# Kernel optimization log

Hardware: AMD Instinct MI355X
Metric: run time of the kernel (lower is better)

## Reference

```python
import jax, jax.numpy as jnp
import numpy as np

N_NODES = 100000
N_EDGES = 1700000  # 1.6M random edges + 100k self-loops (dgl.add_self_loop)
HID = 128
N_GRAPHS = 64
N_CLASSES = 10
T_STEPS = 5


def setup_inputs() -> dict:
    key = jax.random.key(0)
    ks = jax.random.split(key, 12)
    m = jax.random.normal(ks[0], (N_NODES,), dtype=jnp.float32)
    n_rand = N_EDGES - N_NODES
    src_r = jax.random.randint(ks[1], (n_rand,), 0, N_NODES)
    dst_r = jax.random.randint(ks[2], (n_rand,), 0, N_NODES)
    loops = jnp.arange(N_NODES)
    src = jnp.concatenate([src_r, loops])
    dst = jnp.concatenate([dst_r, loops])
    graph_ids = jnp.sort(jax.random.randint(ks[3], (N_NODES,), 0, N_GRAPHS))
    s = 0.05
    W_e = jax.random.normal(ks[4], (HID, HID), dtype=jnp.float32) * s
    b_e = jnp.zeros((HID,), dtype=jnp.float32)
    W_ih = jax.random.normal(ks[5], (3 * HID, HID), dtype=jnp.float32) * s
    b_ih = jnp.zeros((3 * HID,), dtype=jnp.float32)
    W_hh = jax.random.normal(ks[6], (3 * HID, HID), dtype=jnp.float32) * s
    b_hh = jnp.zeros((3 * HID,), dtype=jnp.float32)
    W_cls = jax.random.normal(ks[7], (N_CLASSES, HID), dtype=jnp.float32) * s
    b_cls = jnp.zeros((N_CLASSES,), dtype=jnp.float32)
    return {"m": m, "W_e": W_e, "b_e": b_e, "W_ih": W_ih, "b_ih": b_ih,
            "W_hh": W_hh, "b_hh": b_hh, "W_cls": W_cls, "b_cls": b_cls,
            "src": src, "dst": dst, "graph_ids": graph_ids, "n_graphs": N_GRAPHS}


def _gated_graph_forward(m, W_e, b_e, W_ih, b_ih, W_hh, b_hh, W_cls, b_cls,
                         src, dst, graph_ids, n_graphs):
    n_nodes = m.shape[0]
    hid = W_e.shape[0]
    # h = ndata['m'].view(-1,1), zero-padded to out_feats (DGL GatedGraphConv)
    h = jnp.zeros((n_nodes, hid), dtype=m.dtype).at[:, 0].set(m)
    for _ in range(T_STEPS):
        # single edge type: a[v] = sum_{(u,v) in E} W_e h[u] + b_e
        msg = (h @ W_e.T + b_e)[src]                       # [E, H]
        a = jax.ops.segment_sum(msg, dst, num_segments=n_nodes)
        # torch.nn.GRUCell(a, h); gate order: r, z, n
        gi = a @ W_ih.T + b_ih
        gh = h @ W_hh.T + b_hh
        i_r, i_z, i_n = jnp.split(gi, 3, axis=-1)
        h_r, h_z, h_n = jnp.split(gh, 3, axis=-1)
        r = jax.nn.sigmoid(i_r + h_r)
        z = jax.nn.sigmoid(i_z + h_z)
        n = jnp.tanh(i_n + r * h_n)
        h = (1.0 - z) * n + z * h
    h = jax.nn.relu(h)
    # dgl.mean_nodes: per-graph mean over nodes
    sums = jax.ops.segment_sum(h, graph_ids, num_segments=n_graphs)
    cnt = jax.ops.segment_sum(jnp.ones((n_nodes,), h.dtype), graph_ids,
                              num_segments=n_graphs)
    hg = sums / jnp.maximum(cnt, 1.0)[:, None]             # [G, H]
    return hg @ W_cls.T + b_cls                            # [G, C]


def reference(m, W_e, b_e, W_ih, b_ih, W_hh, b_hh, W_cls, b_cls,
              src, dst, graph_ids, n_graphs):
    return _gated_graph_forward(m, W_e, b_e, W_ih, b_ih, W_hh, b_hh,
                                W_cls, b_cls, src, dst, graph_ids, n_graphs)
```

## Files before the change

kernel.cpp:

```cpp
#include <hip/hip_runtime.h>

#define HID 128
#define G3  384
#define TSTEPS 5
#define BSHIFT 9
#define BNODES (1 << BSHIFT)
#define MAXBUK 256
#define PART_EPB 8192

typedef unsigned int  uint;
typedef unsigned short ushort;

typedef float  f32x4  __attribute__((ext_vector_type(4)));
typedef __bf16 bf16x8 __attribute__((ext_vector_type(8)));

union B8u { uint4 u; bf16x8 b; ushort s[8]; };

static __device__ inline ushort f2bf(float f) {
  uint u = __float_as_uint(f);
  uint r = u + 0x7fffu + ((u >> 16) & 1u);
  return (ushort)(r >> 16);
}
static __device__ inline float bf2f(ushort s) {
  return __uint_as_float(((uint)s) << 16);
}

__global__ __launch_bounds__(128) void k_weights(
    const float* __restrict__ W_e, const float* __restrict__ b_e,
    const float* __restrict__ W_ih, const float* __restrict__ W_hh,
    ushort* __restrict__ Wcomb, ushort* __restrict__ Whh16, float* __restrict__ bvec,
    ushort* __restrict__ Wc0, ushort* __restrict__ Wh0)
{
  int j = blockIdx.x, t = threadIdx.x;
  if (j < G3) {
    __shared__ float row[HID];
    row[t] = W_ih[j * HID + t];
    __syncthreads();
    float acc = 0.f;
    for (int k = 0; k < HID; ++k) acc = fmaf(row[k], W_e[k * HID + t], acc);
    Wcomb[j * HID + t] = f2bf(acc);
    if (t == 0) {
      Wc0[j] = f2bf(acc);
      float b = 0.f;
      for (int k = 0; k < HID; ++k) b += row[k] * b_e[k];
      bvec[j] = b;
    }
  } else {
    int j2 = j - G3;
    Whh16[j2 * HID + t] = f2bf(W_hh[j2 * HID + t]);
    if (t == 0) Wh0[j2] = f2bf(W_hh[j2 * HID]);
  }
}

__global__ __launch_bounds__(256) void k_bh(const int* __restrict__ dst,
                                            int* __restrict__ bhist, int E) {
  __shared__ int lh[MAXBUK];
  int t = threadIdx.x;
  if (t < MAXBUK) lh[t] = 0;
  __syncthreads();
  for (int e = blockIdx.x * 256 + t; e < E; e += gridDim.x * 256)
    atomicAdd(&lh[dst[e] >> BSHIFT], 1);
  __syncthreads();
  if (t < MAXBUK && lh[t]) atomicAdd(&bhist[t], lh[t]);
}

__global__ __launch_bounds__(256) void k_bsc(const int* __restrict__ bhist,
                                             int* __restrict__ bbase,
                                             int* __restrict__ gcur,
                                             int* __restrict__ rowptr, int E, int N) {
  __shared__ int ls[MAXBUK];
  int t = threadIdx.x;
  ls[t] = bhist[t];
  __syncthreads();
  if (t == 0) {
    int run = 0;
    for (int i = 0; i < MAXBUK; ++i) {
      bbase[i] = run; gcur[i] = run; run += ls[i];
    }
    bbase[MAXBUK] = run;
    rowptr[N] = E;
  }
}

__global__ __launch_bounds__(256) void k_part(
    const int* __restrict__ src, const int* __restrict__ dst,
    int* __restrict__ gcur, uint* __restrict__ ebuf, int E) {
  __shared__ int lh[MAXBUK], lbase[MAXBUK], lcur[MAXBUK];
  int t = threadIdx.x;
  int base = blockIdx.x * PART_EPB;
  if (t < MAXBUK) lh[t] = 0;
  __syncthreads();
#pragma unroll 4
  for (int j = 0; j < PART_EPB / 256; ++j) {
    int e = base + j * 256 + t;
    if (e < E) atomicAdd(&lh[dst[e] >> BSHIFT], 1);
  }
  __syncthreads();
  if (t < MAXBUK) {
    lbase[t] = lh[t] ? atomicAdd(&gcur[t], lh[t]) : 0;
    lcur[t] = 0;
  }
  __syncthreads();
#pragma unroll 4
  for (int j = 0; j < PART_EPB / 256; ++j) {
    int e = base + j * 256 + t;
    if (e < E) {
      int d = dst[e];
      int b = d >> BSHIFT;
      int p = atomicAdd(&lcur[b], 1);
      ebuf[lbase[b] + p] = (uint)src[e] | ((uint)(d & (BNODES - 1)) << 20);
    }
  }
}

__global__ __launch_bounds__(256) void k_fill2(
    const uint* __restrict__ ebuf, const int* __restrict__ bbase,
    int* __restrict__ csrc, int* __restrict__ rowptr, int* __restrict__ deg, int N) {
  __shared__ int hcnt[BNODES];
  __shared__ int wls[4];
  int t = threadIdx.x;
  int b = blockIdx.x;
  int ebeg = bbase[b], eend = bbase[b + 1];
  for (int i = t; i < BNODES; i += 256) hcnt[i] = 0;
  __syncthreads();
  for (int e = ebeg + t; e < eend; e += 256)
    atomicAdd(&hcnt[ebuf[e] >> 20], 1);
  __syncthreads();
  const int PER = BNODES / 256;
  int lane = t & 63, wv = t >> 6;
  int x[PER]; int s = 0;
#pragma unroll
  for (int i = 0; i < PER; ++i) { x[i] = hcnt[PER * t + i]; s += x[i]; }
  int incl = s;
#pragma unroll
  for (int off = 1; off < 64; off <<= 1) {
    int u = __shfl_up(incl, off, 64);
    if (lane >= off) incl += u;
  }
  if (lane == 63) wls[wv] = incl;
  __syncthreads();
  int wbase = 0;
  for (int i = 0; i < wv; ++i) wbase += wls[i];
  int run = wbase + incl - s;
#pragma unroll
  for (int i = 0; i < PER; ++i) {
    int node = (b << BSHIFT) + PER * t + i;
    hcnt[PER * t + i] = run;
    if (node < N) { rowptr[node] = ebeg + run; deg[node] = x[i]; }
    run += x[i];
  }
  __syncthreads();
  for (int e = ebeg + t; e < eend; e += 256) {
    uint v = ebuf[e];
    int p = atomicAdd(&hcnt[v >> 20], 1);
    csrc[ebeg + p] = (int)(v & 0xFFFFFu);
  }
}

__global__ void k_minit(const float* __restrict__ m, ushort* __restrict__ m16, int N) {
  int v = blockIdx.x * 256 + threadIdx.x;
  if (v < N) m16[v] = f2bf(m[v]);
}

__global__ __launch_bounds__(256) void k_gather0(
    const int* __restrict__ rowptr, const int* __restrict__ csrc,
    const ushort* __restrict__ m16, ushort* __restrict__ hsum0, int N)
{
  int v = blockIdx.x * 256 + threadIdx.x;
  if (v >= N) return;
  int beg = rowptr[v], end = rowptr[v + 1];
  float a0 = 0.f, a1 = 0.f, a2 = 0.f, a3 = 0.f;
  int e = beg;
  for (; e + 16 <= end; e += 16) {
    a0 += (bf2f(m16[csrc[e + 0]]) + bf2f(m16[csrc[e + 4]])) +
          (bf2f(m16[csrc[e + 8]]) + bf2f(m16[csrc[e + 12]]));
    a1 += (bf2f(m16[csrc[e + 1]]) + bf2f(m16[csrc[e + 5]])) +
          (bf2f(m16[csrc[e + 9]]) + bf2f(m16[csrc[e + 13]]));
    a2 += (bf2f(m16[csrc[e + 2]]) + bf2f(m16[csrc[e + 6]])) +
          (bf2f(m16[csrc[e + 10]]) + bf2f(m16[csrc[e + 14]]));
    a3 += (bf2f(m16[csrc[e + 3]]) + bf2f(m16[csrc[e + 7]])) +
          (bf2f(m16[csrc[e + 11]]) + bf2f(m16[csrc[e + 15]]));
  }
  for (; e < end; e += 4) {
    if (e + 0 < end) a0 += bf2f(m16[csrc[e + 0]]);
    if (e + 1 < end) a1 += bf2f(m16[csrc[e + 1]]);
    if (e + 2 < end) a2 += bf2f(m16[csrc[e + 2]]);
    if (e + 3 < end) a3 += bf2f(m16[csrc[e + 3]]);
  }
  hsum0[v] = f2bf((a0 + a1) + (a2 + a3));
}

__global__ __launch_bounds__(256) void k_gru0(
    const ushort* __restrict__ hsum0, const ushort* __restrict__ m16,
    const int* __restrict__ deg,
    const ushort* __restrict__ Wc0, const ushort* __restrict__ Wh0,
    const float* __restrict__ bvec, const float* __restrict__ b_ih,
    const float* __restrict__ b_hh, ushort* __restrict__ hbn, int N)
{
  int idx = blockIdx.x * 256 + threadIdx.x;
  if (idx >= N * HID) return;
  int n = idx >> 7, d = idx & (HID - 1);
  float s0 = bf2f(hsum0[n]);
  float h0 = bf2f(m16[n]);
  float degf = (float)deg[n];
  float acc0 = s0 * bf2f(Wc0[d]);
  float acc1 = s0 * bf2f(Wc0[d + 128]);
  float acc2 = s0 * bf2f(Wc0[d + 256]);
  float acc3 = h0 * bf2f(Wh0[d]);
  float acc4 = h0 * bf2f(Wh0[d + 128]);
  float acc5 = h0 * bf2f(Wh0[d + 256]);
  float hold = (d == 0) ? h0 : 0.f;
  float ir = acc0 + degf * bvec[d] + b_ih[d];
  float iz = acc1 + degf * bvec[d + 128] + b_ih[d + 128];
  float in_ = acc2 + degf * bvec[d + 256] + b_ih[d + 256];
  float hr = acc3 + b_hh[d];
  float hz = acc4 + b_hh[d + 128];
  float hn = acc5 + b_hh[d + 256];
  float r = __builtin_amdgcn_rcpf(1.f + __expf(-(ir + hr)));
  float z = __builtin_amdgcn_rcpf(1.f + __expf(-(iz + hz)));
  float x2 = in_ + r * hn;
  float e2 = __expf(2.f * x2);
  float nv = 1.f - 2.f * __builtin_amdgcn_rcpf(e2 + 1.f);
  float hv = (1.f - z) * nv + z * hold;
  hbn[idx] = f2bf(hv);
}

static __device__ __forceinline__ void gather_strip(
    const int* __restrict__ rowptr, const int* __restrict__ csrc,
    const ushort* __restrict__ hb, const int* __restrict__ deg,
    int strip, int w, int lane, int N,
    ushort dstS[16][128], ushort dstH[16][128], int* dstDeg)
{
  int node = strip * 16 + w;
  if (node >= N) return;
  int g = lane >> 4;
  int i = lane & 15;
  if (g == 1)
    *(uint4*)(&dstH[w][(i ^ (w & 7)) * 8]) =
        *(const uint4*)(hb + (size_t)node * HID + i * 8);
  if (lane == 32) dstDeg[w] = deg[node];
  int beg = rowptr[node], end = rowptr[node + 1];
  float acc[8] = {0.f, 0.f, 0.f, 0.f, 0.f, 0.f, 0.f, 0.f};
  int e = beg;
  for (; e + 16 <= end; e += 16) {
    int s0 = csrc[e + g];
    int s1 = csrc[e + 4 + g];
    int s2 = csrc[e + 8 + g];
    int s3 = csrc[e + 12 + g];
    B8u w0; w0.u = *(const uint4*)(hb + (size_t)s0 * HID + i * 8);
    B8u w1; w1.u = *(const uint4*)(hb + (size_t)s1 * HID + i * 8);
    B8u w2; w2.u = *(const uint4*)(hb + (size_t)s2 * HID + i * 8);
    B8u w3; w3.u = *(const uint4*)(hb + (size_t)s3 * HID + i * 8);
#pragma unroll
    for (int j = 0; j < 8; ++j)
      acc[j] += (bf2f(w0.s[j]) + bf2f(w1.s[j])) + (bf2f(w2.s[j]) + bf2f(w3.s[j]));
  }
  for (; e < end; e += 4) {
    int ee = e + g;
    if (ee < end) {
      int s0 = csrc[ee];
      B8u wv; wv.u = *(const uint4*)(hb + (size_t)s0 * HID + i * 8);
#pragma unroll
      for (int j = 0; j < 8; ++j) acc[j] += bf2f(wv.s[j]);
    }
  }
#pragma unroll
  for (int j = 0; j < 8; ++j) {
    acc[j] += __shfl_xor(acc[j], 16, 64);
    acc[j] += __shfl_xor(acc[j], 32, 64);
  }
  if (g == 0) {
    uint4 ov;
    ov.x = ((uint)f2bf(acc[1]) << 16) | (uint)f2bf(acc[0]);
    ov.y = ((uint)f2bf(acc[3]) << 16) | (uint)f2bf(acc[2]);
    ov.z = ((uint)f2bf(acc[5]) << 16) | (uint)f2bf(acc[4]);
    ov.w = ((uint)f2bf(acc[7]) << 16) | (uint)f2bf(acc[6]);
    *(uint4*)(&dstS[w][(i ^ (w & 7)) * 8]) = ov;
  }
}

__global__ __launch_bounds__(1024, 4) void k_fused(
    const int* __restrict__ rowptr, const int* __restrict__ csrc,
    const ushort* __restrict__ hbc, ushort* __restrict__ hbn,
    const ushort* __restrict__ Wcomb, const ushort* __restrict__ Whh16,
    const float* __restrict__ bvec, const float* __restrict__ b_ih,
    const float* __restrict__ b_hh, const int* __restrict__ deg, int N)
{
  __shared__ float S[6][16][132];
  __shared__ ushort AT[3][2][16][128];
  __shared__ int degT[3][16];
  const int tid = threadIdx.x;
  const int w = tid >> 6;
  const int lane = tid & 63;
  const int quad = lane >> 4, l16 = lane & 15;
  const int gm = w >> 3;
  const int gw = w & 7;
  const int d0 = gw * 16;

  const ushort* Wmat = gm ? Whh16 : Wcomb;
  B8u bfr[3][4];
#pragma unroll
  for (int g = 0; g < 3; ++g)
#pragma unroll
    for (int kc = 0; kc < 4; ++kc) {
      int j = (d0 + g * 128 + l16) * HID + kc * 32 + quad * 8;
      bfr[g][kc].u = *(const uint4*)(Wmat + j);
    }

  const int ecol = tid & 127, erow0 = tid >> 7;
  const float bir = b_ih[ecol], biz = b_ih[ecol + 128], bin_ = b_ih[ecol + 256];
  const float bhr = b_hh[ecol], bhz = b_hh[ecol + 128], bhn = b_hh[ecol + 256];
  const float vr = bvec[ecol], vz = bvec[ecol + 128], vn = bvec[ecol + 256];

  const int nstrip = N >> 4;
  const int G = (int)gridDim.x;
  int s = blockIdx.x;
  if (s >= nstrip) return;

  gather_strip(rowptr, csrc, hbc, deg, s, w, lane, N, AT[0][0], AT[0][1], degT[0]);
  asm volatile("s_waitcnt lgkmcnt(0)" ::: "memory");
  __builtin_amdgcn_sched_barrier(0);
  __builtin_amdgcn_s_barrier();

  int cur = 0;
  while (true) {
    int ns = s + G;
    bool more = ns < nstrip;
    int nxt = (cur == 2) ? 0 : cur + 1;
    if (more)
      gather_strip(rowptr, csrc, hbc, deg, ns, w, lane, N,
                   AT[nxt][0], AT[nxt][1], degT[nxt]);
    B8u af[4];
#pragma unroll
    for (int kc = 0; kc < 4; ++kc)
      af[kc].u = *(const uint4*)(&AT[cur][gm][l16][(((quad + 4 * kc) ^ (l16 & 7)) * 8)]);
    f32x4 acc[3] = {};
#pragma unroll
    for (int kc = 0; kc < 4; ++kc)
#pragma unroll
      for (int g = 0; g < 3; ++g)
        acc[g] = __builtin_amdgcn_mfma_f32_16x16x32_bf16(af[kc].b, bfr[g][kc].b, acc[g], 0, 0, 0);
    __builtin_amdgcn_s_barrier();
#pragma unroll
    for (int g = 0; g < 3; ++g)
#pragma unroll
      for (int rg = 0; rg < 4; ++rg)
        S[gm * 3 + g][quad * 4 + rg][d0 + l16] = acc[g][rg];
    asm volatile("s_waitcnt lgkmcnt(0)" ::: "memory");
    __builtin_amdgcn_sched_barrier(0);
    __builtin_amdgcn_s_barrier();
    int n0 = s << 4;
#pragma unroll
    for (int k = 0; k < 2; ++k) {
      int row = erow0 + 8 * k;
      float dgf = (float)degT[cur][row];
      int sc = (((ecol >> 3) ^ (row & 7)) * 8) + (ecol & 7);
      float hold = bf2f(AT[cur][1][row][sc]);
      float ir  = S[0][row][ecol] + dgf * vr + bir;
      float iz  = S[1][row][ecol] + dgf * vz + biz;
      float in_ = S[2][row][ecol] + dgf * vn + bin_;
      float hr  = S[3][row][ecol] + bhr;
      float hz  = S[4][row][ecol] + bhz;
      float hn  = S[5][row][ecol] + bhn;
      float r = __builtin_amdgcn_rcpf(1.f + __expf(-(ir + hr)));
      float z = __builtin_amdgcn_rcpf(1.f + __expf(-(iz + hz)));
      float x2 = in_ + r * hn;
      float e2 = __expf(2.f * x2);
      float nv = 1.f - 2.f * __builtin_amdgcn_rcpf(e2 + 1.f);
      float hv = (1.f - z) * nv + z * hold;
      hbn[(size_t)(n0 + row) * HID + ecol] = f2bf(hv);
    }
    if (!more) break;
    s = ns; cur = nxt;
  }
}

__global__ __launch_bounds__(64) void k_bounds(const int* __restrict__ gid,
                                               int* __restrict__ cnt, int N, int G) {
  int g = threadIdx.x;
  if (g >= G) return;
  int lo = 0, hi = N;
  while (lo < hi) { int mid = (lo + hi) >> 1; if (gid[mid] < g) lo = mid + 1; else hi = mid; }
  int lb0 = lo;
  lo = 0; hi = N;
  int g1 = g + 1;
  while (lo < hi) { int mid = (lo + hi) >> 1; if (gid[mid] < g1) lo = mid + 1; else hi = mid; }
  cnt[g] = lo - lb0;
}

#define POOL_CHUNK 96
__global__ __launch_bounds__(128) void k_pool(const ushort* __restrict__ hb,
                                              const int* __restrict__ gid,
                                              float* __restrict__ hg, int N) {
  int d = threadIdx.x;
  int start = blockIdx.x * POOL_CHUNK;
  if (start >= N) return;
  int end = min(start + POOL_CHUNK, N);
  float acc = 0.f;
  int g = gid[start];
  for (int n = start; n < end; ++n) {
    int gn = gid[n];
    if (gn != g) { unsafeAtomicAdd(&hg[g * HID + d], acc); acc = 0.f; g = gn; }
    acc += fmaxf(bf2f(hb[(size_t)n * HID + d]), 0.f);
  }
  unsafeAtomicAdd(&hg[g * HID + d], acc);
}

__global__ __launch_bounds__(640) void k_cls(const float* __restrict__ hg,
                                             const int* __restrict__ cnt,
                                             const float* __restrict__ Wc,
                                             const float* __restrict__ bc,
                                             float* __restrict__ out, int G) {
  int t = threadIdx.x;
  if (t >= G * 10) return;
  int g = t / 10, c = t % 10;
  float inv = 1.f / fmaxf((float)cnt[g], 1.f);
  float acc = 0.f;
  for (int d = 0; d < HID; ++d) acc = fmaf(hg[g * HID + d], Wc[c * HID + d], acc);
  out[t] = acc * inv + bc[c];
}

extern "C" void kernel_launch(void* const* d_in, const int* in_sizes, int n_in,
                              void* d_out, int out_size, void* d_ws, size_t ws_size,
                              hipStream_t stream) {
  const int N = in_sizes[0];
  const int E = in_sizes[9];
  const float* m    = (const float*)d_in[0];
  const float* W_e  = (const float*)d_in[1];
  const float* b_e  = (const float*)d_in[2];
  const float* W_ih = (const float*)d_in[3];
  const float* b_ih = (const float*)d_in[4];
  const float* W_hh = (const float*)d_in[5];
  const float* b_hh = (const float*)d_in[6];
  const float* W_cls = (const float*)d_in[7];
  const float* b_cls = (const float*)d_in[8];
  const int* src = (const int*)d_in[9];
  const int* dst = (const int*)d_in[10];
  const int* gid = (const int*)d_in[11];
  const int G = out_size / 10;
  float* out = (float*)d_out;

  size_t off = 0;
  auto alloc = [&](size_t b) {
    char* p = (char*)d_ws + off;
    off += (b + 255) & ~(size_t)255;
    return (void*)p;
  };
  ushort* hb0    = (ushort*)alloc((size_t)N * HID * 2);
  ushort* hb1    = (ushort*)alloc((size_t)N * HID * 2);
  int*    deg    = (int*)   alloc((size_t)N * 4);
  int*    rowptr = (int*)   alloc((size_t)(N + 1) * 4);
  int*    csrc   = (int*)   alloc((size_t)E * 4);
  uint*   ebuf   = (uint*)  alloc((size_t)E * 4);
  int*    bhist  = (int*)   alloc((size_t)MAXBUK * 4);
  int*    bbase  = (int*)   alloc((size_t)(MAXBUK + 1) * 4);
  int*    gcur   = (int*)   alloc((size_t)MAXBUK * 4);
  ushort* Wcomb  = (ushort*)alloc((size_t)G3 * HID * 2);
  ushort* Whh16  = (ushort*)alloc((size_t)G3 * HID * 2);
  float*  bvec   = (float*) alloc((size_t)G3 * 4);
  float*  hg     = (float*) alloc((size_t)G * HID * 4);
  int*    cnt    = (int*)   alloc((size_t)G * 4);
  ushort* m16    = (ushort*)alloc((size_t)N * 2);
  ushort* hsum0  = (ushort*)alloc((size_t)N * 2);
  ushort* Wc0    = (ushort*)alloc((size_t)G3 * 2);
  ushort* Wh0    = (ushort*)alloc((size_t)G3 * 2);
  if (off > ws_size) return;

  const int NBUK = (N + BNODES - 1) >> BSHIFT;

  k_weights<<<2 * G3, HID, 0, stream>>>(W_e, b_e, W_ih, W_hh, Wcomb, Whh16, bvec, Wc0, Wh0);
  k_minit<<<(N + 255) / 256, 256, 0, stream>>>(m, m16, N);
  hipMemsetAsync(bhist, 0, (size_t)MAXBUK * 4, stream);
  k_bh<<<256, 256, 0, stream>>>(dst, bhist, E);
  k_bsc<<<1, MAXBUK, 0, stream>>>(bhist, bbase, gcur, rowptr, E, N);
  k_part<<<(E + PART_EPB - 1) / PART_EPB, 256, 0, stream>>>(src, dst, gcur, ebuf, E);
  k_fill2<<<NBUK, 256, 0, stream>>>(ebuf, bbase, csrc, rowptr, deg, N);

  k_gather0<<<(N + 255) / 256, 256, 0, stream>>>(rowptr, csrc, m16, hsum0, N);
  k_gru0<<<(N * HID + 255) / 256, 256, 0, stream>>>(hsum0, m16, deg, Wc0, Wh0,
                                                    bvec, b_ih, b_hh, hb1, N);

  ushort* hbc = hb1;
  ushort* hbn = hb0;
  const int nstrip = N >> 4;
  const int fuse_blocks = nstrip < 256 ? nstrip : 256;
  for (int s = 1; s < TSTEPS; ++s) {
    k_fused<<<fuse_blocks, 1024, 0, stream>>>(rowptr, csrc, hbc, hbn,
                                              Wcomb, Whh16, bvec, b_ih, b_hh, deg, N);
    ushort* t = hbc; hbc = hbn; hbn = t;
  }

  hipMemsetAsync(hg, 0, (size_t)G * HID * 4, stream);
  k_bounds<<<1, 64, 0, stream>>>(gid, cnt, N, G);
  k_pool<<<(N + POOL_CHUNK - 1) / POOL_CHUNK, HID, 0, stream>>>(hbc, gid, hg, N);
  k_cls<<<1, 640, 0, stream>>>(hg, cnt, W_cls, b_cls, out, G);
}
```

Baseline: 795.5 us.

## Prefetch neighbor rows two strips ahead via async global-to-LDS loads

Replaces the per-strip gather call with an inline two-stage pipeline. Edge indices and up to 16 neighbor rows for the strip two iterations ahead are issued early as direct global-to-LDS loads into a per-wave staging buffer. Those rows are consumed one iteration later, and high-degree nodes fall back to a 4x-unrolled register gather. It also moves the nine bias vectors into LDS to free registers. The goal is to hide gather latency behind the MFMA and GRU work, at the cost of about 64KB more LDS, which may reduce occupancy below the launch-bound target.

```diff
diff --git a/kernel.cpp b/kernel.cpp
--- a/kernel.cpp
+++ b/kernel.cpp
@@ -23,6 +23,12 @@
 }
 static __device__ inline float bf2f(ushort s) {
   return __uint_as_float(((uint)s) << 16);
+}
+
+static __device__ __forceinline__ void gload_lds16(const void* g, void* l) {
+  __builtin_amdgcn_global_load_lds(
+      (const __attribute__((address_space(1))) uint*)g,
+      (__attribute__((address_space(3))) uint*)l, 16, 0, 0);
 }
 
 __global__ __launch_bounds__(128) void k_weights(
@@ -289,6 +295,8 @@
   __shared__ float S[6][16][132];
   __shared__ ushort AT[3][2][16][128];
   __shared__ int degT[3][16];
+  __shared__ ushort STG[16][2048];
+  __shared__ float BL[9][128];
   const int tid = threadIdx.x;
   const int w = tid >> 6;
   const int lane = tid & 63;
@@ -296,82 +304,196 @@
   const int gm = w >> 3;
   const int gw = w & 7;
   const int d0 = gw * 16;
+  const int g = lane >> 4, i = lane & 15;
 
   const ushort* Wmat = gm ? Whh16 : Wcomb;
   B8u bfr[3][4];
 #pragma unroll
-  for (int g = 0; g < 3; ++g)
+  for (int gg = 0; gg < 3; ++gg)
 #pragma unroll
     for (int kc = 0; kc < 4; ++kc) {
-      int j = (d0 + g * 128 + l16) * HID + kc * 32 + quad * 8;
-      bfr[g][kc].u = *(const uint4*)(Wmat + j);
-    }
+      int j = (d0 + gg * 128 + l16) * HID + kc * 32 + quad * 8;
+      bfr[gg][kc].u = *(const uint4*)(Wmat + j);
+    }
+
+  for (int kk = tid; kk < 9 * 128; kk += 1024) {
+    int grp = kk >> 7, col = kk & 127;
+    const float* sp = (grp < 3) ? b_ih : (grp < 6 ? b_hh : bvec);
+    BL[grp][col] = sp[(grp % 3) * 128 + col];
+  }
 
   const int ecol = tid & 127, erow0 = tid >> 7;
-  const float bir = b_ih[ecol], biz = b_ih[ecol + 128], bin_ = b_ih[ecol + 256];
-  const float bhr = b_hh[ecol], bhz = b_hh[ecol + 128], bhn = b_hh[ecol + 256];
-  const float vr = bvec[ecol], vz = bvec[ecol + 128], vn = bvec[ecol + 256];
-
   const int nstrip = N >> 4;
   const int G = (int)gridDim.x;
-  int s = blockIdx.x;
-  if (s >= nstrip) return;
-
-  gather_strip(rowptr, csrc, hbc, deg, s, w, lane, N, AT[0][0], AT[0][1], degT[0]);
+  const int t0 = blockIdx.x;
+  if (t0 >= nstrip) return;
+
+  gather_strip(rowptr, csrc, hbc, deg, t0, w, lane, N, AT[0][0], AT[0][1], degT[0]);
+  int idx[7]; int cnt = 0; int beg = 0;
+  if (t0 + G < nstrip) {
+    int node = (t0 + G) * 16 + w;
+    beg = rowptr[node]; int end = rowptr[node + 1]; cnt = end - beg;
+#pragma unroll
+    for (int j = 0; j < 7; ++j) { int ee = beg + 4 * j + g; idx[j] = (ee < end) ? csrc[ee] : 0; }
+    if (cnt <= 28) {
+#pragma unroll
+      for (int j = 0; j < 4; ++j)
+        if (4 * j + g < cnt)
+          gload_lds16(hbc + (size_t)idx[j] * HID + i * 8, &STG[w][j * 512]);
+    }
+  }
   asm volatile("s_waitcnt lgkmcnt(0)" ::: "memory");
   __builtin_amdgcn_sched_barrier(0);
   __builtin_amdgcn_s_barrier();
 
-  int cur = 0;
+  int k = 0;
   while (true) {
-    int ns = s + G;
-    bool more = ns < nstrip;
-    int nxt = (cur == 2) ? 0 : cur + 1;
-    if (more)
-      gather_strip(rowptr, csrc, hbc, deg, ns, w, lane, N,
-                   AT[nxt][0], AT[nxt][1], degT[nxt]);
+    const int scur = t0 + k * G;
+    const int cur = k % 3;
+    const int s1 = scur + G;
+    const bool have1 = (s1 < nstrip);
+    const int nxt = (k + 1) % 3;
+
+    if (have1) {
+      int node = s1 * 16 + w;
+      asm volatile("s_waitcnt vmcnt(0)" ::: "memory");
+      __builtin_amdgcn_sched_barrier(0);
+      uint4 hrow = make_uint4(0, 0, 0, 0);
+      if (g == 1) hrow = *(const uint4*)(hbc + (size_t)node * HID + i * 8);
+      int dgv = 0;
+      if (lane == 32) dgv = deg[node];
+      float acc[8] = {0.f, 0.f, 0.f, 0.f, 0.f, 0.f, 0.f, 0.f};
+      if (cnt > 28) {
+        int end = beg + cnt;
+        int e = beg;
+        for (; e + 16 <= end; e += 16) {
+          int s0 = csrc[e + g];
+          int sa = csrc[e + 4 + g];
+          int sb = csrc[e + 8 + g];
+          int sc2 = csrc[e + 12 + g];
+          B8u w0; w0.u = *(const uint4*)(hbc + (size_t)s0 * HID + i * 8);
+          B8u w1; w1.u = *(const uint4*)(hbc + (size_t)sa * HID + i * 8);
+          B8u w2; w2.u = *(const uint4*)(hbc + (size_t)sb * HID + i * 8);
+          B8u w3; w3.u = *(const uint4*)(hbc + (size_t)sc2 * HID + i * 8);
+#pragma unroll
+          for (int j = 0; j < 8; ++j)
+            acc[j] += (bf2f(w0.s[j]) + bf2f(w1.s[j])) + (bf2f(w2.s[j]) + bf2f(w3.s[j]));
+        }
+        for (; e < end; e += 4) {
+          int ee = e + g;
+          if (ee < end) {
+            int s0 = csrc[ee];
+            B8u wv; wv.u = *(const uint4*)(hbc + (size_t)s0 * HID + i * 8);
+#pragma unroll
+            for (int j = 0; j < 8; ++j) acc[j] += bf2f(wv.s[j]);
+          }
+        }
+      } else if (cnt >= 16) {
+        B8u r0, r1, r2, r3;
+        r0.u = *(const uint4*)&STG[w][0 * 512 + lane * 8];
+        r1.u = *(const uint4*)&STG[w][1 * 512 + lane * 8];
+        r2.u = *(const uint4*)&STG[w][2 * 512 + lane * 8];
+        r3.u = *(const uint4*)&STG[w][3 * 512 + lane * 8];
+#pragma unroll
+        for (int j = 0; j < 8; ++j)
+          acc[j] += (bf2f(r0.s[j]) + bf2f(r1.s[j])) + (bf2f(r2.s[j]) + bf2f(r3.s[j]));
+#pragma unroll
+        for (int jj = 4; jj < 7; ++jj)
+          if (4 * jj + g < cnt) {
+            B8u rv; rv.u = *(const uint4*)(hbc + (size_t)idx[jj] * HID + i * 8);
+#pragma unroll
+            for (int j = 0; j < 8; ++j) acc[j] += bf2f(rv.s[j]);
+          }
+      } else {
+#pragma unroll
+        for (int jj = 0; jj < 4; ++jj)
+          if (4 * jj + g < cnt) {
+            B8u rv; rv.u = *(const uint4*)&STG[w][jj * 512 + lane * 8];
+#pragma unroll
+            for (int j = 0; j < 8; ++j) acc[j] += bf2f(rv.s[j]);
+          }
+      }
+#pragma unroll
+      for (int j = 0; j < 8; ++j) {
+        acc[j] += __shfl_xor(acc[j], 16, 64);
+        acc[j] += __shfl_xor(acc[j], 32, 64);
+      }
+      if (g == 0) {
+        uint4 ov;
+        ov.x = ((uint)f2bf(acc[1]) << 16) | (uint)f2bf(acc[0]);
+        ov.y = ((uint)f2bf(acc[3]) << 16) | (uint)f2bf(acc[2]);
+        ov.z = ((uint)f2bf(acc[5]) << 16) | (uint)f2bf(acc[4]);
+        ov.w = ((uint)f2bf(acc[7]) << 16) | (uint)f2bf(acc[6]);
+        *(uint4*)(&AT[nxt][0][w][(i ^ (w & 7)) * 8]) = ov;
+      }
+      if (g == 1) *(uint4*)(&AT[nxt][1][w][(i ^ (w & 7)) * 8]) = hrow;
+      if (lane == 32) degT[nxt][w] = dgv;
+    }
+
+    {
+      int s2 = scur + 2 * G;
+      if (s2 < nstrip) {
+        __builtin_amdgcn_sched_barrier(0);
+        int node2 = s2 * 16 + w;
+        beg = rowptr[node2]; int end = rowptr[node2 + 1]; cnt = end - beg;
+#pragma unroll
+        for (int j = 0; j < 7; ++j) { int ee = beg + 4 * j + g; idx[j] = (ee < end) ? csrc[ee] : 0; }
+        if (cnt <= 28) {
+#pragma unroll
+          for (int j = 0; j < 4; ++j)
+            if (4 * j + g < cnt)
+              gload_lds16(hbc + (size_t)idx[j] * HID + i * 8, &STG[w][j * 512]);
+        }
+      } else cnt = 0;
+    }
+
     B8u af[4];
 #pragma unroll
     for (int kc = 0; kc < 4; ++kc)
       af[kc].u = *(const uint4*)(&AT[cur][gm][l16][(((quad + 4 * kc) ^ (l16 & 7)) * 8)]);
-    f32x4 acc[3] = {};
+    f32x4 acc3[3] = {};
 #pragma unroll
     for (int kc = 0; kc < 4; ++kc)
 #pragma unroll
-      for (int g = 0; g < 3; ++g)
-        acc[g] = __builtin_amdgcn_mfma_f32_16x16x32_bf16(af[kc].b, bfr[g][kc].b, acc[g], 0, 0, 0);
+      for (int gg = 0; gg < 3; ++gg)
+        acc3[gg] = __builtin_amdgcn_mfma_f32_16x16x32_bf16(af[kc].b, bfr[gg][kc].b, acc3[gg], 0, 0, 0);
     __builtin_amdgcn_s_barrier();
 #pragma unroll
-    for (int g = 0; g < 3; ++g)
+    for (int gg = 0; gg < 3; ++gg)
 #pragma unroll
       for (int rg = 0; rg < 4; ++rg)
-        S[gm * 3 + g][quad * 4 + rg][d0 + l16] = acc[g][rg];
+        S[gm * 3 + gg][quad * 4 + rg][d0 + l16] = acc3[gg][rg];
     asm volatile("s_waitcnt lgkmcnt(0)" ::: "memory");
     __builtin_amdgcn_sched_barrier(0);
     __builtin_amdgcn_s_barrier();
-    int n0 = s << 4;
-#pragma unroll
-    for (int k = 0; k < 2; ++k) {
-      int row = erow0 + 8 * k;
-      float dgf = (float)degT[cur][row];
-      int sc = (((ecol >> 3) ^ (row & 7)) * 8) + (ecol & 7);
-      float hold = bf2f(AT[cur][1][row][sc]);
-      float ir  = S[0][row][ecol] + dgf * vr + bir;
-      float iz  = S[1][row][ecol] + dgf * vz + biz;
-      float in_ = S[2][row][ecol] + dgf * vn + bin_;
-      float hr  = S[3][row][ecol] + bhr;
-      float hz  = S[4][row][ecol] + bhz;
-      float hn  = S[5][row][ecol] + bhn;
-      float r = __builtin_amdgcn_rcpf(1.f + __expf(-(ir + hr)));
-      float z = __builtin_amdgcn_rcpf(1.f + __expf(-(iz + hz)));
-      float x2 = in_ + r * hn;
-      float e2 = __expf(2.f * x2);
-      float nv = 1.f - 2.f * __builtin_amdgcn_rcpf(e2 + 1.f);
-      float hv = (1.f - z) * nv + z * hold;
-      hbn[(size_t)(n0 + row) * HID + ecol] = f2bf(hv);
-    }
-    if (!more) break;
-    s = ns; cur = nxt;
+    {
+      float bir = BL[0][ecol], biz = BL[1][ecol], bin_ = BL[2][ecol];
+      float bhr = BL[3][ecol], bhz = BL[4][ecol], bhn = BL[5][ecol];
+      float vr = BL[6][ecol], vz = BL[7][ecol], vn = BL[8][ecol];
+      int n0 = scur << 4;
+#pragma unroll
+      for (int kk = 0; kk < 2; ++kk) {
+        int row = erow0 + 8 * kk;
+        float dgf = (float)degT[cur][row];
+        int sc = (((ecol >> 3) ^ (row & 7)) * 8) + (ecol & 7);
+        float hold = bf2f(AT[cur][1][row][sc]);
+        float ir  = S[0][row][ecol] + dgf * vr + bir;
+        float iz  = S[1][row][ecol] + dgf * vz + biz;
+        float in_ = S[2][row][ecol] + dgf * vn + bin_;
+        float hr  = S[3][row][ecol] + bhr;
+        float hz  = S[4][row][ecol] + bhz;
+        float hn  = S[5][row][ecol] + bhn;
+        float r = __builtin_amdgcn_rcpf(1.f + __expf(-(ir + hr)));
+        float z = __builtin_amdgcn_rcpf(1.f + __expf(-(iz + hz)));
+        float x2 = in_ + r * hn;
+        float e2 = __expf(2.f * x2);
+        float nv = 1.f - 2.f * __builtin_amdgcn_rcpf(e2 + 1.f);
+        float hv = (1.f - z) * nv + z * hold;
+        hbn[(size_t)(n0 + row) * HID + ecol] = f2bf(hv);
+      }
+    }
+    if (!have1) break;
+    ++k;
   }
 }
 
```

New measurement: 814.7 us. +2.4%, slower.
